# Performance work log

Hardware: AMD Instinct MI355X
Metric: run time of the kernel (lower is better)

Reference implementation:

```python
import jax, jax.numpy as jnp
import numpy as np


def setup_inputs() -> dict:
    key = jax.random.key(0)
    k1, k2, k3 = jax.random.split(key, 3)
    B, C, H, W = 4, 16, 64, 64
    F, K = 32, 3
    x = jax.random.normal(k1, (B, C, H, W), dtype=jnp.float32)
    # Pade coefficients per (out_channel, in_channel, a, b): numerator deg 5, denom deg 4.
    nums = jax.random.normal(k2, (F, C, K, K, 6), dtype=jnp.float32) * 0.3
    denoms = jax.random.normal(k3, (F, C, K, K, 4), dtype=jnp.float32) * 0.3
    return {"x": x, "nums": nums, "denoms": denoms}


def _rational_conv(x, nums, denoms):
    B, C, H, W = x.shape
    F, _, K, _, _ = nums.shape
    p = (K - 1) // 2
    # pad spatially, move channels last: (B, H+2p, W+2p, C)
    xp = jnp.pad(x, ((0, 0), (0, 0), (p, p), (p, p))).transpose(0, 2, 3, 1)
    # im2col patches: stack the K*K shifted views -> (B, H, W, K2, C)
    patches = jnp.stack(
        [xp[:, a:a + H, b:b + W, :] for a in range(K) for b in range(K)], axis=3
    )
    # powers x^0..x^5 built by repeated multiply (safe for negative bases)
    pws = [jnp.ones_like(patches)]
    for _ in range(5):
        pws.append(pws[-1] * patches)
    pw = jnp.stack(pws, axis=-1)                         # (B,H,W,K2,C,6)
    nums_r = nums.reshape(F, C, K * K, 6)                # (a,b) flattened a*K+b, matches patch order
    denoms_r = denoms.reshape(F, C, K * K, 4)
    # P(x) = sum_n a_n x^n ; Q(x) = 1 + |sum_m b_m x^m|, m=1..4  (Pade version A)
    P = jnp.einsum('bhwkcn,fckn->bhwfkc', pw, nums_r)
    Q = 1.0 + jnp.abs(jnp.einsum('bhwkcm,fckm->bhwfkc', pw[..., 1:5], denoms_r))
    out = (P / Q).sum(axis=(4, 5))                       # (B,H,W,F)
    return out.transpose(0, 3, 1, 2)                     # (B,F,H,W)


def reference(x, nums, denoms):
    return _rational_conv(x, nums, denoms)
```

## Files before the change

### kernel.cpp

```cpp
#include <hip/hip_runtime.h>

#define B_ 4
#define C_ 16
#define H_ 64
#define W_ 64
#define F_ 32
#define S_ 66
#define CH_ (S_ * S_)
#define NPAD_ (B_ * C_ * CH_)

__global__ __launch_bounds__(256)
void pad_kernel(const float* __restrict__ x, float* __restrict__ xp) {
    const int i  = blockIdx.x * 256 + threadIdx.x;
    const int cc = i % S_;
    const int t  = i / S_;
    const int r  = t % S_;
    const int bc = t / S_;
    float v = 0.f;
    if (r >= 1 && r <= H_ && cc >= 1 && cc <= W_)
        v = x[(size_t)bc * (H_ * W_) + (r - 1) * W_ + (cc - 1)];
    xp[i] = v;
}

__global__ __launch_bounds__(256)
void ka_rconv_kernel(const float* __restrict__ xp,
                     const float* __restrict__ nums,
                     const float* __restrict__ denoms,
                     float* __restrict__ out) {
    __shared__ float red[2 * 2 * 64];

    const int tid = threadIdx.x;
    const int col = tid & 63;
    const int g   = (tid >> 6) & 1;
    const int rp  = tid >> 7;

    int bid = blockIdx.x;
    const int f  = bid & 31;  bid >>= 5;
    const int t4 = bid & 15;  bid >>= 4;
    const int b  = bid;
    const int gy0 = t4 * 4 + rp * 2;

    const int c0 = __builtin_amdgcn_readfirstlane(g * 8);

    const float* nbase = nums   + ((size_t)f * C_ + c0) * 54;
    const float* dbase = denoms + ((size_t)f * C_ + c0) * 36;
    const float* xb = xp + ((size_t)(b * C_ + c0)) * CH_ + gy0 * S_ + col;

    float acc0 = 0.f, acc1 = 0.f;
    float3 A[4], Bv[4];

    auto loadrows = [&](float3* dst, const float* p) {
        #pragma unroll
        for (int a = 0; a < 4; ++a)
            dst[a] = *(const float3*)(p + a * S_);
    };

    auto evalch = [&](const float3* rv, int c) {
        const float* np = nbase + c * 54;
        const float* dp = dbase + c * 36;
        #pragma unroll
        for (int a = 0; a < 3; ++a) {
            #pragma unroll
            for (int j = 0; j < 3; ++j) {
                const int t = a * 3 + j;
                const float x0 = (j == 0) ? rv[a].x     : (j == 1) ? rv[a].y     : rv[a].z;
                const float x1 = (j == 0) ? rv[a + 1].x : (j == 1) ? rv[a + 1].y : rv[a + 1].z;
                const float n0 = np[t*6+0], n1 = np[t*6+1], n2 = np[t*6+2];
                const float n3 = np[t*6+3], n4 = np[t*6+4], n5 = np[t*6+5];
                const float d0 = dp[t*4+0], d1 = dp[t*4+1], d2 = dp[t*4+2], d3 = dp[t*4+3];

                float P0 = fmaf(n5, x0, n4), P1 = fmaf(n5, x1, n4);
                P0 = fmaf(P0, x0, n3);  P1 = fmaf(P1, x1, n3);
                P0 = fmaf(P0, x0, n2);  P1 = fmaf(P1, x1, n2);
                P0 = fmaf(P0, x0, n1);  P1 = fmaf(P1, x1, n1);
                P0 = fmaf(P0, x0, n0);  P1 = fmaf(P1, x1, n0);

                float Q0 = fmaf(d3, x0, d2), Q1 = fmaf(d3, x1, d2);
                Q0 = fmaf(Q0, x0, d1);  Q1 = fmaf(Q1, x1, d1);
                Q0 = fmaf(Q0, x0, d0);  Q1 = fmaf(Q1, x1, d0);
                Q0 *= x0;               Q1 *= x1;
                Q0 = 1.0f + fabsf(Q0);  Q1 = 1.0f + fabsf(Q1);

                acc0 = fmaf(P0, __builtin_amdgcn_rcpf(Q0), acc0);
                acc1 = fmaf(P1, __builtin_amdgcn_rcpf(Q1), acc1);
            }
        }
    };

    loadrows(A, xb);
    const float* pa = xb;
    const float* pb = xb + CH_;
    #pragma unroll 1
    for (int c = 0; c < 8; c += 2) {
        loadrows(Bv, pb);
        evalch(A, c);
        pa += 2 * CH_;
        if (c + 2 < 8) loadrows(A, pa);
        evalch(Bv, c + 1);
        pb += 2 * CH_;
    }

    if (g == 1) {
        red[(rp * 2 + 0) * 64 + col] = acc0;
        red[(rp * 2 + 1) * 64 + col] = acc1;
    }
    __syncthreads();
    if (g == 0) {
        acc0 += red[(rp * 2 + 0) * 64 + col];
        acc1 += red[(rp * 2 + 1) * 64 + col];
        float* op = out + (((size_t)b * F_ + f) * H_ + gy0) * W_ + col;
        op[0]  = acc0;
        op[W_] = acc1;
    }
}

extern "C" void kernel_launch(void* const* d_in, const int* in_sizes, int n_in,
                              void* d_out, int out_size, void* d_ws, size_t ws_size,
                              hipStream_t stream) {
    const float* x      = (const float*)d_in[0];
    const float* nums   = (const float*)d_in[1];
    const float* denoms = (const float*)d_in[2];
    float* outp = (float*)d_out;
    float* xpad = (float*)d_ws;

    pad_kernel<<<NPAD_ / 256, 256, 0, stream>>>(x, xpad);
    dim3 grid(B_ * 16 * F_);
    ka_rconv_kernel<<<grid, 256, 0, stream>>>(xpad, nums, denoms, outp);
}
```

Before: 84.25 us.

## Stage Pade coefficients in LDS and drop manual double-buffered row loads

Each block now cooperatively copies its output channel's numerator and denominator coefficients into shared memory, padded to 12 floats per tap so each tap reads them with vector LDS loads. Before, coefficients came through wave-uniform scalar global loads. The software double-buffering of input rows across channel pairs is removed in favour of a plain per-channel loop. This adds a global-to-LDS copy and a barrier per block, and moves coefficient traffic from the scalar unit onto the vector LDS path, which competes with the ALU work. Losing the explicit prefetch may also expose global-load latency.

Measured after the change: 83.20 us. About the same (-1.2%).

```diff
diff --git a/kernel.cpp b/kernel.cpp
--- a/kernel.cpp
+++ b/kernel.cpp
@@ -8,6 +8,7 @@
 #define S_ 66
 #define CH_ (S_ * S_)
 #define NPAD_ (B_ * C_ * CH_)
+#define CST 12
 
 __global__ __launch_bounds__(256)
 void pad_kernel(const float* __restrict__ x, float* __restrict__ xp) {
@@ -27,6 +28,7 @@
                      const float* __restrict__ nums,
                      const float* __restrict__ denoms,
                      float* __restrict__ out) {
+    __shared__ alignas(16) float sc[C_ * 9 * CST];
     __shared__ float red[2 * 2 * 64];
 
     const int tid = threadIdx.x;
@@ -40,64 +42,58 @@
     const int b  = bid;
     const int gy0 = t4 * 4 + rp * 2;
 
-    const int c0 = __builtin_amdgcn_readfirstlane(g * 8);
+    {
+        const float* np = nums + (size_t)f * (C_ * 54);
+        for (int i = tid; i < C_ * 54; i += 256) {
+            int e = i / 6, j = i - e * 6;
+            sc[e * CST + j] = np[i];
+        }
+        const float* dp = denoms + (size_t)f * (C_ * 36);
+        for (int i = tid; i < C_ * 36; i += 256) {
+            int e = i / 4, j = i - e * 4;
+            sc[e * CST + 6 + j] = dp[i];
+        }
+    }
+    __syncthreads();
 
-    const float* nbase = nums   + ((size_t)f * C_ + c0) * 54;
-    const float* dbase = denoms + ((size_t)f * C_ + c0) * 36;
-    const float* xb = xp + ((size_t)(b * C_ + c0)) * CH_ + gy0 * S_ + col;
+    const int chb = g * 8;
+    const float* xb = xp + ((size_t)(b * C_ + chb)) * CH_ + gy0 * S_ + col;
+    const float* cp = sc + chb * (9 * CST);
 
     float acc0 = 0.f, acc1 = 0.f;
-    float3 A[4], Bv[4];
 
-    auto loadrows = [&](float3* dst, const float* p) {
+    for (int c = 0; c < 8; ++c) {
+        const float* xr = xb + c * CH_;
+        float3 rv[4];
         #pragma unroll
         for (int a = 0; a < 4; ++a)
-            dst[a] = *(const float3*)(p + a * S_);
-    };
+            rv[a] = *(const float3*)(xr + a * S_);
 
-    auto evalch = [&](const float3* rv, int c) {
-        const float* np = nbase + c * 54;
-        const float* dp = dbase + c * 36;
+        const float* ce = cp + c * (9 * CST);
         #pragma unroll
-        for (int a = 0; a < 3; ++a) {
-            #pragma unroll
-            for (int j = 0; j < 3; ++j) {
-                const int t = a * 3 + j;
-                const float x0 = (j == 0) ? rv[a].x     : (j == 1) ? rv[a].y     : rv[a].z;
-                const float x1 = (j == 0) ? rv[a + 1].x : (j == 1) ? rv[a + 1].y : rv[a + 1].z;
-                const float n0 = np[t*6+0], n1 = np[t*6+1], n2 = np[t*6+2];
-                const float n3 = np[t*6+3], n4 = np[t*6+4], n5 = np[t*6+5];
-                const float d0 = dp[t*4+0], d1 = dp[t*4+1], d2 = dp[t*4+2], d3 = dp[t*4+3];
+        for (int t = 0; t < 9; ++t) {
+            const float4 k0 = *(const float4*)(ce + t * CST);
+            const float4 k1 = *(const float4*)(ce + t * CST + 4);
+            const float2 k2 = *(const float2*)(ce + t * CST + 8);
+            const int a = t / 3, j = t % 3;
+            const float x0 = (j == 0) ? rv[a].x     : (j == 1) ? rv[a].y     : rv[a].z;
+            const float x1 = (j == 0) ? rv[a + 1].x : (j == 1) ? rv[a + 1].y : rv[a + 1].z;
 
-                float P0 = fmaf(n5, x0, n4), P1 = fmaf(n5, x1, n4);
-                P0 = fmaf(P0, x0, n3);  P1 = fmaf(P1, x1, n3);
-                P0 = fmaf(P0, x0, n2);  P1 = fmaf(P1, x1, n2);
-                P0 = fmaf(P0, x0, n1);  P1 = fmaf(P1, x1, n1);
-                P0 = fmaf(P0, x0, n0);  P1 = fmaf(P1, x1, n0);
+            float P0 = fmaf(k1.y, x0, k1.x), P1 = fmaf(k1.y, x1, k1.x);
+            P0 = fmaf(P0, x0, k0.w);  P1 = fmaf(P1, x1, k0.w);
+            P0 = fmaf(P0, x0, k0.z);  P1 = fmaf(P1, x1, k0.z);
+            P0 = fmaf(P0, x0, k0.y);  P1 = fmaf(P1, x1, k0.y);
+            P0 = fmaf(P0, x0, k0.x);  P1 = fmaf(P1, x1, k0.x);
 
-                float Q0 = fmaf(d3, x0, d2), Q1 = fmaf(d3, x1, d2);
-                Q0 = fmaf(Q0, x0, d1);  Q1 = fmaf(Q1, x1, d1);
-                Q0 = fmaf(Q0, x0, d0);  Q1 = fmaf(Q1, x1, d0);
-                Q0 *= x0;               Q1 *= x1;
-                Q0 = 1.0f + fabsf(Q0);  Q1 = 1.0f + fabsf(Q1);
+            float Q0 = fmaf(k2.y, x0, k2.x), Q1 = fmaf(k2.y, x1, k2.x);
+            Q0 = fmaf(Q0, x0, k1.w);  Q1 = fmaf(Q1, x1, k1.w);
+            Q0 = fmaf(Q0, x0, k1.z);  Q1 = fmaf(Q1, x1, k1.z);
+            Q0 *= x0;                 Q1 *= x1;
+            Q0 = 1.0f + fabsf(Q0);    Q1 = 1.0f + fabsf(Q1);
 
-                acc0 = fmaf(P0, __builtin_amdgcn_rcpf(Q0), acc0);
-                acc1 = fmaf(P1, __builtin_amdgcn_rcpf(Q1), acc1);
-            }
+            acc0 = fmaf(P0, __builtin_amdgcn_rcpf(Q0), acc0);
+            acc1 = fmaf(P1, __builtin_amdgcn_rcpf(Q1), acc1);
         }
-    };
-
-    loadrows(A, xb);
-    const float* pa = xb;
-    const float* pb = xb + CH_;
-    #pragma unroll 1
-    for (int c = 0; c < 8; c += 2) {
-        loadrows(Bv, pb);
-        evalch(A, c);
-        pa += 2 * CH_;
-        if (c + 2 < 8) loadrows(A, pa);
-        evalch(Bv, c + 1);
-        pb += 2 * CH_;
     }
 
     if (g == 1) {
```
